# Optimization experiments

Measured on AMD Instinct MI355X. Metric: run time of the kernel, lower is better.

The kernel has to match this reference:

```python
import jax, jax.numpy as jnp
import numpy as np

D_IN, D_K, D_V = 1024, 1024, 1024
B, S = 4, 2048

def setup_inputs() -> dict:
    key = jax.random.key(0)
    ks = jax.random.split(key, 7)
    s = 1.0 / np.sqrt(D_IN)
    return {
        "x": jax.random.normal(ks[0], (B, S, D_IN), dtype=jnp.float32),
        "Wq": jax.random.uniform(ks[1], (D_IN, D_K), jnp.float32, -s, s),
        "bq": jax.random.uniform(ks[2], (D_K,), jnp.float32, -s, s),
        "Wk": jax.random.uniform(ks[3], (D_IN, D_K), jnp.float32, -s, s),
        "bk": jax.random.uniform(ks[4], (D_K,), jnp.float32, -s, s),
        "Wv": jax.random.uniform(ks[5], (D_IN, D_V), jnp.float32, -s, s),
        "bv": jax.random.uniform(ks[6], (D_V,), jnp.float32, -s, s),
    }

def reference(x, Wq, bq, Wk, bk, Wv, bv):
    # QKV projections: [B,S,d_in] @ [d_in,d] + b
    Q = x @ Wq + bq  # [B,S,d_k]
    K = x @ Wk + bk  # [B,S,d_k]
    V = x @ Wv + bv  # [B,S,d_v]
    # Non-standard recipe: softmax over UNSCALED scores, then divide output by sqrt(d_k)
    scores = jnp.einsum('bqd,bkd->bqk', Q, K)  # [B,S,S]
    attn = jax.nn.softmax(scores, axis=2)
    out = jnp.einsum('bqk,bkv->bqv', attn, V) / jnp.sqrt(jnp.asarray(K.shape[2], dtype=x.dtype))
    return out
```

## Files before the change

### kernel.cpp

```cpp
#include <hip/hip_runtime.h>
#include <stdint.h>

typedef unsigned short u16;
typedef _Float16 f16;
typedef _Float16 f16x8 __attribute__((ext_vector_type(8)));
typedef float f32x4 __attribute__((ext_vector_type(4)));

#define DIN 1024
#define SEQ 2048
#define NB 4
#define MB (1u << 20)


__device__ __forceinline__ void gload_lds16(const void* g, void* l) {
    __builtin_amdgcn_global_load_lds(
        (__attribute__((address_space(1))) void*)(uintptr_t)g,
        (__attribute__((address_space(3))) void*)l,
        16, 0, 0);
}

__device__ __forceinline__ int xcd_swz(int h, int cpx) {
    return (h & 7) * cpx + (h >> 3);
}

__device__ __forceinline__ void barrier_raw() {
    asm volatile("" ::: "memory");
    __builtin_amdgcn_s_barrier();
    asm volatile("" ::: "memory");
}
__device__ __forceinline__ void lgkm0() {
    asm volatile("s_waitcnt lgkmcnt(0)" ::: "memory");
    __builtin_amdgcn_sched_barrier(0);
}
template<int N>
__device__ __forceinline__ void wait_vm() {
    asm volatile("s_waitcnt vmcnt(%0)" :: "i"(N) : "memory");
}


__device__ __forceinline__ void gemm256(
    const char* __restrict__ A, const char* __restrict__ B,
    int ldab, int ldbb, int nt, char* smem, f32x4 acc[8][4])
{
    const int tid  = threadIdx.x;
    const int lane = tid & 63;
    const int wave = tid >> 6;
    const int ln15 = lane & 15;
    const int k16  = (lane >> 4) << 4;
    const int wmB  = (wave >> 2) * 128;
    const int wnB  = (wave & 3) * 64;

    #pragma unroll
    for (int m = 0; m < 8; ++m)
        #pragma unroll
        for (int n = 0; n < 4; ++n)
            acc[m][n] = (f32x4){0.f, 0.f, 0.f, 0.f};

    const char* pA[2];
    const char* pB[2];
    #pragma unroll
    for (int i = 0; i < 2; ++i) {
        const int La = i * 8192 + tid * 16;
        const int r  = La >> 7;
        const int sc = (La & 127) ^ ((r & 7) << 4);
        pA[i] = A + (size_t)r * ldab + sc;
        pB[i] = B + (size_t)r * ldbb + sc;
    }
    const int ldsw = wave * 1024;

    f16x8 a[4][2], b[4][2];

    auto stage = [&](int g) {
        if (g < 4 * nt) {
            const int ks  = g >> 2;
            const int isB = ((g & 2) == 0);
            const int h   = g & 1;
            char* l = smem + (ks & 1) * 65536 + (isB ? 32768 : 0) + h * 16384 + ldsw;
            #pragma unroll
            for (int i = 0; i < 2; ++i) {
                const char* gp = (isB ? pB[i] + (size_t)(h * 128) * ldbb
                                      : pA[i] + (size_t)(h * 128) * ldab) + ks * 128;
                gload_lds16(gp, l + i * 8192);
            }
        }
    };

#define RDA(qm) { _Pragma("unroll") for (int mf = 0; mf < 4; ++mf) { \
        const int r = wmB + ((qm) * 4 + mf) * 16 + ln15; \
        const int sw = (r & 7) << 4; \
        const char* p = sAc + r * 128; \
        a[mf][0] = *(const f16x8*)(p + ((k16) ^ sw)); \
        a[mf][1] = *(const f16x8*)(p + ((64 + k16) ^ sw)); } }

#define RDB() { _Pragma("unroll") for (int nf = 0; nf < 4; ++nf) { \
        const int r = wnB + nf * 16 + ln15; \
        const int sw = (r & 7) << 4; \
        const char* p = sBc + r * 128; \
        b[nf][0] = *(const f16x8*)(p + ((k16) ^ sw)); \
        b[nf][1] = *(const f16x8*)(p + ((64 + k16) ^ sw)); } }

#define MM(qm, nf0) { __builtin_amdgcn_s_setprio(1); \
        _Pragma("unroll") for (int mf = 0; mf < 4; ++mf) \
        _Pragma("unroll") for (int nf = (nf0); nf < (nf0) + 2; ++nf) { \
            acc[(qm)*4+mf][nf] = __builtin_amdgcn_mfma_f32_16x16x32_f16( \
                a[mf][0], b[nf][0], acc[(qm)*4+mf][nf], 0, 0, 0); \
            acc[(qm)*4+mf][nf] = __builtin_amdgcn_mfma_f32_16x16x32_f16( \
                a[mf][1], b[nf][1], acc[(qm)*4+mf][nf], 0, 0, 0); } \
        __builtin_amdgcn_s_setprio(0); }

    #pragma unroll
    for (int g = 0; g < 8; ++g) stage(g);
    wait_vm<8>();
    barrier_raw();

    for (int t = 0; t < nt; ++t) {
        const char* sAc = smem + (t & 1) * 65536;
        const char* sBc = sAc + 32768;
        const int gb = 4 * (t + 2);
        RDA(0); RDB();
        barrier_raw(); lgkm0(); MM(0, 0); barrier_raw();
        stage(gb + 0);
        barrier_raw(); MM(0, 2); barrier_raw();
        RDA(1); stage(gb + 1);
        barrier_raw(); lgkm0(); MM(1, 0); barrier_raw();
        stage(gb + 2); stage(gb + 3);
        if (t < nt - 2) { wait_vm<8>(); } else if (t == nt - 2) { wait_vm<0>(); }
        barrier_raw(); MM(1, 2); barrier_raw();
    }
#undef RDA
#undef RDB
#undef MM
}


__device__ __forceinline__ void gemm_tile(
    const char* __restrict__ A, const char* __restrict__ B,
    int lda, int ldb, int ksteps, char* smem, f32x4 acc[4][4])
{
    const int lane = threadIdx.x & 63;
    const int wave = threadIdx.x >> 6;

    #pragma unroll
    for (int m = 0; m < 4; ++m)
        #pragma unroll
        for (int n = 0; n < 4; ++n)
            acc[m][n] = (f32x4){0.f, 0.f, 0.f, 0.f};

    const char* ga[4];
    const char* gb[4];
    int ldsoff[4];
    #pragma unroll
    for (int i = 0; i < 4; ++i) {
        int La = (wave * 4 + i) * 1024 + lane * 16;
        int r  = La >> 7;
        int cb = La & 127;
        int sc = cb ^ ((r & 7) << 4);
        ga[i] = A + (size_t)r * (size_t)(lda * 2) + sc;
        gb[i] = B + (size_t)r * (size_t)(ldb * 2) + sc;
        ldsoff[i] = (wave * 4 + i) * 1024;
    }

    const int wr = (wave >> 1) * 64;
    const int wc = (wave & 1) * 64;

    for (int ks = 0; ks < ksteps; ++ks) {
        #pragma unroll
        for (int i = 0; i < 4; ++i) {
            gload_lds16(ga[i], smem + ldsoff[i]);
            gload_lds16(gb[i], smem + 16384 + ldsoff[i]);
            ga[i] += 128;
            gb[i] += 128;
        }
        __syncthreads();

        #pragma unroll
        for (int kk = 0; kk < 2; ++kk) {
            const int kb = kk * 64 + ((lane >> 4) << 4);
            f16x8 af[4], bfv[4];
            #pragma unroll
            for (int m = 0; m < 4; ++m) {
                int r = wr + m * 16 + (lane & 15);
                af[m] = *(const f16x8*)(smem + r * 128 + (kb ^ ((r & 7) << 4)));
            }
            #pragma unroll
            for (int n = 0; n < 4; ++n) {
                int r = wc + n * 16 + (lane & 15);
                bfv[n] = *(const f16x8*)(smem + 16384 + r * 128 + (kb ^ ((r & 7) << 4)));
            }
            #pragma unroll
            for (int m = 0; m < 4; ++m)
                #pragma unroll
                for (int n = 0; n < 4; ++n)
                    acc[m][n] = __builtin_amdgcn_mfma_f32_16x16x32_f16(
                        af[m], bfv[n], acc[m][n], 0, 0, 0);
        }
        __syncthreads();
    }
}


__global__ __launch_bounds__(256) void k_prep(
    const float* __restrict__ x, f16* __restrict__ xh,
    const float* __restrict__ Wq, const float* __restrict__ Wk,
    const float* __restrict__ Wv, f16* __restrict__ wt)
{
    __shared__ float tile[32][33];
    const int bid = blockIdx.x;
    if (bid < 2048) {
        const int n8 = (NB * SEQ * DIN) / 8;
        for (int idx = bid * 256 + threadIdx.x; idx < n8; idx += 2048 * 256) {
            f32x4 a = ((const f32x4*)x)[(size_t)idx * 2];
            f32x4 b = ((const f32x4*)x)[(size_t)idx * 2 + 1];
            f16x8 o;
            o[0] = (f16)a[0]; o[1] = (f16)a[1]; o[2] = (f16)a[2]; o[3] = (f16)a[3];
            o[4] = (f16)b[0]; o[5] = (f16)b[1]; o[6] = (f16)b[2]; o[7] = (f16)b[3];
            ((f16x8*)xh)[idx] = o;
        }
    } else {
        const int wb = bid - 2048;
        const int mtx = wb >> 10;
        const int rem = wb & 1023;
        const int n0 = (rem & 31) * 32, k0 = (rem >> 5) * 32;
        const float* W = (mtx == 0) ? Wq : (mtx == 1 ? Wk : Wv);
        const int c = threadIdx.x & 31, r0 = threadIdx.x >> 5;
        #pragma unroll
        for (int rr = r0; rr < 32; rr += 8)
            tile[rr][c] = W[(size_t)(k0 + rr) * DIN + n0 + c];
        __syncthreads();
        f16* o = wt + (size_t)mtx * DIN * DIN;
        #pragma unroll
        for (int rr = r0; rr < 32; rr += 8)
            o[(size_t)(n0 + rr) * DIN + k0 + c] = (f16)tile[c][rr];
    }
}

__global__ __launch_bounds__(512, 2) void k_gemm_qkv8(
    const f16* __restrict__ xh, const f16* __restrict__ wt,
    const float* __restrict__ bq, const float* __restrict__ bk,
    const float* __restrict__ bv,
    f16* __restrict__ Q, f16* __restrict__ K, f16* __restrict__ Vt)
{
    extern __shared__ char smem[];
    f32x4 acc[8][4];
    const int sid = xcd_swz(blockIdx.x, 48);
    const int blkN = sid % 12;
    const int blkM = sid / 12;
    gemm256((const char*)(xh + (size_t)blkM * 256 * DIN),
            (const char*)(wt + (size_t)blkN * 256 * DIN),
            DIN * 2, DIN * 2, DIN / 64, smem, acc);

    const int lane = threadIdx.x & 63;
    const int wave = threadIdx.x >> 6;
    const int row0 = blkM * 256 + (wave >> 2) * 128;
    const int col0 = blkN * 256 + (wave & 3) * 64;

    if (col0 >= 2048) {
        const int bb = row0 >> 11;
        const int sb = row0 & (SEQ - 1);
        f16* Vtb = Vt + (size_t)bb * DIN * SEQ;
        #pragma unroll
        for (int n = 0; n < 4; ++n) {
            int d = (col0 - 2048) + n * 16 + (lane & 15);
            float bias = bv[d];
            #pragma unroll
            for (int m = 0; m < 8; ++m) {
                #pragma unroll
                for (int j = 0; j < 4; ++j) {
                    int s = sb + m * 16 + (lane >> 4) * 4 + j;
                    Vtb[(size_t)d * SEQ + s] = (f16)(acc[m][n][j] + bias);
                }
            }
        }
    } else {
        f16* dst = (col0 < 1024) ? Q : K;
        const float* bsrc = (col0 < 1024) ? bq : bk;
        const int ncb = col0 & 1023;
        #pragma unroll
        for (int n = 0; n < 4; ++n) {
            int nc = ncb + n * 16 + (lane & 15);
            float bias = bsrc[nc];
            #pragma unroll
            for (int m = 0; m < 8; ++m) {
                #pragma unroll
                for (int j = 0; j < 4; ++j) {
                    int row = row0 + m * 16 + (lane >> 4) * 4 + j;
                    dst[(size_t)row * 1024 + nc] = (f16)(acc[m][n][j] + bias);
                }
            }
        }
    }
}

__global__ __launch_bounds__(512, 2) void k_gemm_scores8(
    const f16* __restrict__ Q, const f16* __restrict__ K, float* __restrict__ S)
{
    extern __shared__ char smem[];
    f32x4 acc[8][4];
    const int sid = xcd_swz(blockIdx.x, 32);
    const int bx = sid & 7, by = (sid >> 3) & 7, b = sid >> 6;
    const f16* Qb = Q + (size_t)b * SEQ * DIN;
    const f16* Kb = K + (size_t)b * SEQ * DIN;
    gemm256((const char*)(Qb + (size_t)by * 256 * DIN),
            (const char*)(Kb + (size_t)bx * 256 * DIN),
            DIN * 2, DIN * 2, DIN / 64, smem, acc);

    float* Sb = S + (size_t)b * SEQ * SEQ;
    const int lane = threadIdx.x & 63;
    const int wave = threadIdx.x >> 6;
    const int row0 = by * 256 + (wave >> 2) * 128;
    const int col0 = bx * 256 + (wave & 3) * 64;
    #pragma unroll
    for (int m = 0; m < 8; ++m)
        #pragma unroll
        for (int n = 0; n < 4; ++n) {
            int col = col0 + n * 16 + (lane & 15);
            #pragma unroll
            for (int j = 0; j < 4; ++j) {
                int row = row0 + m * 16 + (lane >> 4) * 4 + j;
                Sb[(size_t)row * SEQ + col] = acc[m][n][j];
            }
        }
}

__global__ __launch_bounds__(256) void k_softmax(
    const float* __restrict__ S, f16* __restrict__ P)
{
    const size_t row = blockIdx.x;
    const float* s = S + row * SEQ;
    f16* p = P + row * SEQ;
    const int t = threadIdx.x;

    f32x4 x0 = ((const f32x4*)s)[t * 2];
    f32x4 x1 = ((const f32x4*)s)[t * 2 + 1];
    float v[8] = {x0[0], x0[1], x0[2], x0[3], x1[0], x1[1], x1[2], x1[3]};

    float mx = v[0];
    #pragma unroll
    for (int j = 1; j < 8; ++j) mx = fmaxf(mx, v[j]);
    #pragma unroll
    for (int o = 32; o; o >>= 1) mx = fmaxf(mx, __shfl_xor(mx, o, 64));
    __shared__ float red[8];
    if ((t & 63) == 0) red[t >> 6] = mx;
    __syncthreads();
    mx = fmaxf(fmaxf(red[0], red[1]), fmaxf(red[2], red[3]));

    float sum = 0.f;
    #pragma unroll
    for (int j = 0; j < 8; ++j) { v[j] = __expf(v[j] - mx); sum += v[j]; }
    #pragma unroll
    for (int o = 32; o; o >>= 1) sum += __shfl_xor(sum, o, 64);
    if ((t & 63) == 0) red[4 + (t >> 6)] = sum;
    __syncthreads();
    sum = (red[4] + red[5]) + (red[6] + red[7]);
    float inv = 1.0f / sum;

    f16x8 o8;
    #pragma unroll
    for (int j = 0; j < 8; ++j) o8[j] = (f16)(v[j] * inv);
    ((f16x8*)p)[t] = o8;
}

__global__ __launch_bounds__(256) void k_gemm_pv(
    const f16* __restrict__ P, const f16* __restrict__ Vt, float* __restrict__ out)
{
    __shared__ __align__(16) char smem[32768];
    f32x4 acc[4][4];
    const int sid = xcd_swz(blockIdx.x, 64);
    const int bx = sid & 7;
    const int by = (sid >> 3) & 15;
    const int b  = sid >> 7;
    const f16* Pb  = P  + (size_t)b * SEQ * SEQ;
    const f16* Vtb = Vt + (size_t)b * 1024 * SEQ;
    gemm_tile((const char*)(Pb  + (size_t)by * 128 * SEQ),
              (const char*)(Vtb + (size_t)bx * 128 * SEQ),
              SEQ, SEQ, SEQ / 64, smem, acc);

    float* ob = out + (size_t)b * SEQ * 1024;
    const int lane = threadIdx.x & 63;
    const int wave = threadIdx.x >> 6;
    const int row0 = by * 128 + (wave >> 1) * 64;
    const int col0 = bx * 128 + (wave & 1) * 64;
    #pragma unroll
    for (int m = 0; m < 4; ++m)
        #pragma unroll
        for (int n = 0; n < 4; ++n) {
            int col = col0 + n * 16 + (lane & 15);
            #pragma unroll
            for (int j = 0; j < 4; ++j) {
                int row = row0 + m * 16 + (lane >> 4) * 4 + j;
                ob[(size_t)row * 1024 + col] = acc[m][n][j] * 0.03125f;
            }
        }
}


extern "C" void kernel_launch(void* const* d_in, const int* in_sizes, int n_in,
                              void* d_out, int out_size, void* d_ws, size_t ws_size,
                              hipStream_t stream) {
    const float* x  = (const float*)d_in[0];
    const float* Wq = (const float*)d_in[1];
    const float* bq = (const float*)d_in[2];
    const float* Wk = (const float*)d_in[3];
    const float* bk = (const float*)d_in[4];
    const float* Wv = (const float*)d_in[5];
    const float* bv = (const float*)d_in[6];
    float* out = (float*)d_out;
    char* ws = (char*)d_ws;

    f16*  Q  = (f16*)(ws);
    f16*  K  = (f16*)(ws + (size_t)16 * MB);
    f16*  Vt = (f16*)(ws + (size_t)32 * MB);
    f16*  xh = (f16*)(ws + (size_t)48 * MB);
    f16*  wt = (f16*)(ws + (size_t)64 * MB);
    float* S = (float*)(ws + (size_t)48 * MB);
    f16*  P  = Q;

    const size_t needed = (size_t)112 * MB;
    if (ws_size < needed) return;

    hipFuncSetAttribute((const void*)k_gemm_qkv8,
                        hipFuncAttributeMaxDynamicSharedMemorySize, 131072);
    hipFuncSetAttribute((const void*)k_gemm_scores8,
                        hipFuncAttributeMaxDynamicSharedMemorySize, 131072);

    k_prep<<<5120, 256, 0, stream>>>(x, xh, Wq, Wk, Wv, wt);
    k_gemm_qkv8<<<384, 512, 131072, stream>>>(xh, wt, bq, bk, bv, Q, K, Vt);
    k_gemm_scores8<<<256, 512, 131072, stream>>>(Q, K, S);
    k_softmax<<<NB * SEQ, 256, 0, stream>>>(S, P);
    k_gemm_pv<<<512, 256, 0, stream>>>(P, Vt, out);
}
```

Before: 177.7 us.

## Double-buffer A fragments and prefetch next tile's A rows during MFMA

Splits A register fragments into two buffers (a0/a1) so the next k-step's first A half is read from LDS while the current step's last MFMA block runs, and B reads are split into two halves with partial lgkmcnt waits. The goal is to hide LDS read latency behind matrix ops instead of stalling on lgkmcnt(0). The global stage ordering and vmcnt waits are reshuffled to match. This costs extra VGPRs for the second A buffer, which may lower occupancy, and it reads the next buffer before the barrier that guards its load.

```diff
diff --git a/kernel.cpp b/kernel.cpp
--- a/kernel.cpp
+++ b/kernel.cpp
@@ -28,8 +28,9 @@
     __builtin_amdgcn_s_barrier();
     asm volatile("" ::: "memory");
 }
-__device__ __forceinline__ void lgkm0() {
-    asm volatile("s_waitcnt lgkmcnt(0)" ::: "memory");
+template<int N>
+__device__ __forceinline__ void wait_lgkm() {
+    asm volatile("s_waitcnt lgkmcnt(%0)" :: "i"(N) : "memory");
     __builtin_amdgcn_sched_barrier(0);
 }
 template<int N>
@@ -68,7 +69,7 @@
     }
     const int ldsw = wave * 1024;
 
-    f16x8 a[4][2], b[4][2];
+    f16x8 a0[4][2], a1[4][2], b[4][2];
 
     auto stage = [&](int g) {
         if (g < 4 * nt) {
@@ -85,50 +86,67 @@
         }
     };
 
-#define RDA(qm) { _Pragma("unroll") for (int mf = 0; mf < 4; ++mf) { \
-        const int r = wmB + ((qm) * 4 + mf) * 16 + ln15; \
+#define RDA0(base) { _Pragma("unroll") for (int mf = 0; mf < 4; ++mf) { \
+        const int r = wmB + mf * 16 + ln15; \
         const int sw = (r & 7) << 4; \
-        const char* p = sAc + r * 128; \
-        a[mf][0] = *(const f16x8*)(p + ((k16) ^ sw)); \
-        a[mf][1] = *(const f16x8*)(p + ((64 + k16) ^ sw)); } }
-
-#define RDB() { _Pragma("unroll") for (int nf = 0; nf < 4; ++nf) { \
+        const char* p = (base) + r * 128; \
+        a0[mf][0] = *(const f16x8*)(p + (k16 ^ sw)); \
+        a0[mf][1] = *(const f16x8*)(p + ((64 + k16) ^ sw)); } }
+
+#define RDA1(base) { _Pragma("unroll") for (int mf = 0; mf < 4; ++mf) { \
+        const int r = wmB + (mf + 4) * 16 + ln15; \
+        const int sw = (r & 7) << 4; \
+        const char* p = (base) + r * 128; \
+        a1[mf][0] = *(const f16x8*)(p + (k16 ^ sw)); \
+        a1[mf][1] = *(const f16x8*)(p + ((64 + k16) ^ sw)); } }
+
+#define RDB2(nf0, base) { _Pragma("unroll") for (int nf = (nf0); nf < (nf0) + 2; ++nf) { \
         const int r = wnB + nf * 16 + ln15; \
         const int sw = (r & 7) << 4; \
-        const char* p = sBc + r * 128; \
-        b[nf][0] = *(const f16x8*)(p + ((k16) ^ sw)); \
+        const char* p = (base) + r * 128; \
+        b[nf][0] = *(const f16x8*)(p + (k16 ^ sw)); \
         b[nf][1] = *(const f16x8*)(p + ((64 + k16) ^ sw)); } }
 
-#define MM(qm, nf0) { __builtin_amdgcn_s_setprio(1); \
+#define MM(aa, aoff, nf0) { __builtin_amdgcn_s_setprio(1); \
         _Pragma("unroll") for (int mf = 0; mf < 4; ++mf) \
         _Pragma("unroll") for (int nf = (nf0); nf < (nf0) + 2; ++nf) { \
-            acc[(qm)*4+mf][nf] = __builtin_amdgcn_mfma_f32_16x16x32_f16( \
-                a[mf][0], b[nf][0], acc[(qm)*4+mf][nf], 0, 0, 0); \
-            acc[(qm)*4+mf][nf] = __builtin_amdgcn_mfma_f32_16x16x32_f16( \
-                a[mf][1], b[nf][1], acc[(qm)*4+mf][nf], 0, 0, 0); } \
+            acc[(aoff) + mf][nf] = __builtin_amdgcn_mfma_f32_16x16x32_f16( \
+                aa[mf][0], b[nf][0], acc[(aoff) + mf][nf], 0, 0, 0); \
+            acc[(aoff) + mf][nf] = __builtin_amdgcn_mfma_f32_16x16x32_f16( \
+                aa[mf][1], b[nf][1], acc[(aoff) + mf][nf], 0, 0, 0); } \
         __builtin_amdgcn_s_setprio(0); }
 
     #pragma unroll
     for (int g = 0; g < 8; ++g) stage(g);
     wait_vm<8>();
     barrier_raw();
+    RDA0(smem);
 
     for (int t = 0; t < nt; ++t) {
         const char* sAc = smem + (t & 1) * 65536;
         const char* sBc = sAc + 32768;
+        const char* sAn = smem + ((t + 1) & 1) * 65536;
         const int gb = 4 * (t + 2);
-        RDA(0); RDB();
-        barrier_raw(); lgkm0(); MM(0, 0); barrier_raw();
-        stage(gb + 0);
-        barrier_raw(); MM(0, 2); barrier_raw();
-        RDA(1); stage(gb + 1);
-        barrier_raw(); lgkm0(); MM(1, 0); barrier_raw();
+
+        RDB2(0, sBc);
+        __builtin_amdgcn_sched_barrier(0);
+        RDB2(2, sBc);
+        barrier_raw(); wait_lgkm<4>(); MM(a0, 0, 0); barrier_raw();
+
+        RDA1(sAc);
+        barrier_raw(); wait_lgkm<8>(); MM(a0, 0, 2); barrier_raw();
+
+        stage(gb + 0); stage(gb + 1);
+        if (t < nt - 2) { wait_vm<4>(); } else if (t == nt - 2) { wait_vm<0>(); }
+        barrier_raw(); wait_lgkm<0>(); MM(a1, 4, 0); barrier_raw();
+
+        RDA0(sAn);
         stage(gb + 2); stage(gb + 3);
-        if (t < nt - 2) { wait_vm<8>(); } else if (t == nt - 2) { wait_vm<0>(); }
-        barrier_raw(); MM(1, 2); barrier_raw();
-    }
-#undef RDA
-#undef RDB
+        barrier_raw(); MM(a1, 4, 2); barrier_raw();
+    }
+#undef RDA0
+#undef RDA1
+#undef RDB2
 #undef MM
 }
 
```

Result: no change. 176.1 us (-0.9%).
